# Optimization experiments

Hardware: AMD Instinct MI355X
Metric: run time of the kernel (lower is better)

The kernel has to match this reference:

```python
import jax, jax.numpy as jnp
import numpy as np

NEG_SLOPE = 0.2  # PyG GATConv default negative_slope


def _gat_layer(x, src, dst, n_nodes, W, a_src, a_dst, b):
    # x: [N, din]; src/dst: [E] (self-loops already included)
    h = x @ W                                  # [N, dout]
    s_src = h @ a_src                          # [N]
    s_dst = h @ a_dst                          # [N]
    e = jax.nn.leaky_relu(s_src[src] + s_dst[dst], NEG_SLOPE)  # [E]
    # per-target-node softmax over incoming edges (stable via segment max)
    m = jax.ops.segment_max(e, dst, num_segments=n_nodes)      # [N]
    a = jnp.exp(e - m[dst])                    # [E]
    denom = jax.ops.segment_sum(a, dst, num_segments=n_nodes)  # [N]
    msg = h[src] * a[:, None]                  # [E, dout]
    agg = jax.ops.segment_sum(msg, dst, num_segments=n_nodes)  # [N, dout]
    return agg / denom[:, None] + b


def setup_inputs() -> dict:
    key = jax.random.key(0)
    ks = jax.random.split(key, 16)
    N, E = 100000, 1600000
    in_dim, hid_dim, out_dim = 128, 128, 64
    x = jax.random.normal(ks[0], (N, in_dim), dtype=jnp.float32)
    edge_idx = jax.random.randint(ks[1], (2, E), 0, N, dtype=jnp.int32)

    def lin(k, din, dout):
        return jax.random.normal(k, (din, dout), dtype=jnp.float32) * (1.0 / np.sqrt(din))

    def att(k, dout):
        return jax.random.normal(k, (dout,), dtype=jnp.float32) * (1.0 / np.sqrt(dout))

    return {
        "x": x, "edge_idx": edge_idx,
        "W1": lin(ks[2], in_dim, hid_dim), "as1": att(ks[3], hid_dim), "ad1": att(ks[4], hid_dim), "b1": jnp.zeros((hid_dim,), jnp.float32),
        "W2": lin(ks[5], hid_dim, hid_dim), "as2": att(ks[6], hid_dim), "ad2": att(ks[7], hid_dim), "b2": jnp.zeros((hid_dim,), jnp.float32),
        "W3": lin(ks[8], hid_dim, out_dim), "as3": att(ks[9], out_dim), "ad3": att(ks[10], out_dim), "b3": jnp.zeros((out_dim,), jnp.float32),
    }


def reference(x, edge_idx, W1, as1, ad1, b1, W2, as2, ad2, b2, W3, as3, ad3, b3):
    N = x.shape[0]
    # add self-loops (PyG GATConv default add_self_loops=True)
    loops = jnp.arange(N, dtype=edge_idx.dtype)
    src = jnp.concatenate([edge_idx[0], loops])
    dst = jnp.concatenate([edge_idx[1], loops])
    h = _gat_layer(x, src, dst, N, W1, as1, ad1, b1)
    h = _gat_layer(h, src, dst, N, W2, as2, ad2, b2)
    h = _gat_layer(h, src, dst, N, W3, as3, ad3, b3)
    return jnp.mean(h, axis=-2)  # [out_dim]
```

## Files before the change

kernel.cpp:

```cpp
#include <hip/hip_runtime.h>

static inline int ceil_div(long long a, long long b) { return (int)((a + b - 1) / b); }

typedef __attribute__((ext_vector_type(8))) short bf16x8;
typedef __attribute__((ext_vector_type(4))) float f32x4;

#define TILE 8192
#define BKSH 9

__device__ __forceinline__ float lrelu(float t) { return t > 0.f ? t : 0.2f * t; }

__device__ __forceinline__ void atomAddF(float* p, float v) {
  unsafeAtomicAdd(p, v);
}

__device__ __forceinline__ unsigned int f2bf(float f) {
  unsigned int u = __float_as_uint(f);
  unsigned int r = ((u >> 16) & 1u) + 0x7fffu;
  return (u + r) >> 16;
}

__device__ __forceinline__ void gll16(const void* g, void* l) {
  __builtin_amdgcn_global_load_lds((const __attribute__((address_space(1))) void*)g,
                                   (__attribute__((address_space(3))) void*)l, 16, 0, 0);
}

__global__ void prep(const float* __restrict__ W1, const float* __restrict__ W2,
                     const float* __restrict__ W3, unsigned short* __restrict__ Wt1,
                     unsigned short* __restrict__ Wt2, unsigned short* __restrict__ Wt3,
                     int* __restrict__ tot, float* __restrict__ dout, int NBUK) {
  const int j = blockIdx.x * blockDim.x + threadIdx.x;
  if (j < 40960) {
    const float* W; unsigned short* Wt; int local, DOUTv;
    if (j < 16384)      { W = W1; Wt = Wt1; local = j;          DOUTv = 128; }
    else if (j < 32768) { W = W2; Wt = Wt2; local = j - 16384;  DOUTv = 128; }
    else                { W = W3; Wt = Wt3; local = j - 32768;  DOUTv = 64;  }
    const int k = local / DOUTv, n = local % DOUTv;
    Wt[n * 128 + k] = (unsigned short)f2bf(W[local]);
    return;
  }
  const int z = j - 40960;
  if (z < NBUK) tot[z] = 0;
  else if (z < NBUK + 64) dout[z - NBUK] = 0.f;
}

template<int DOUT, bool XF32>
__launch_bounds__(256)
__global__ void gemm_mfma(const unsigned short* __restrict__ Xb, const float* __restrict__ xf,
                          const unsigned short* __restrict__ Wt,
                          const float* __restrict__ avs, const float* __restrict__ avd,
                          unsigned short* __restrict__ Hb, float* __restrict__ Ss,
                          float* __restrict__ Sd, int N, int RG) {
  constexpr int DIN = 128;
  constexpr int CG = DOUT / 64;
  constexpr int RPB = 4 / CG;
  constexpr int SPSR = (CG == 2) ? RPB : 1;
  constexpr int CHR = DOUT / 4;
  constexpr int SWM = CHR / 8;
  constexpr int XR  = RPB * 64;

  __shared__ float sps[SPSR][2][64], spd[SPSR][2][64];
  __shared__ uint4 smem4[(DOUT + XR) * 16];
  unsigned short* sWt = (unsigned short*)smem4;
  unsigned short* sXb = (unsigned short*)smem4 + DOUT * DIN;
  unsigned int*   sO32 = (unsigned int*)smem4;

  const int tid = threadIdx.x;
  const int wv = tid >> 6;
  const int rgl = wv / CG;
  const int cg  = wv % CG;
  const int rg = blockIdx.x * RPB + rgl;
  const bool active = rg < RG;
  const int lane = tid & 63;
  const int l16 = lane & 15, quad = lane >> 4;
  const int row0 = rg * 64, colw0 = cg * 64;
  const int row0blk = blockIdx.x * XR;

#pragma unroll
  for (int i = 0; i < DOUT / 16; i++) {
    const int r4 = wv * (DOUT / 4) + i * 4;
    const int r = r4 + (lane >> 4);
    const int ch = (lane & 15) ^ (r & 7);
    gll16(Wt + (size_t)r * DIN + ch * 8, sWt + (size_t)r4 * DIN);
  }
  if (XF32) {
    for (int c = tid; c < XR * 16; c += 256) {
      const int row = c >> 4, ch = c & 15;
      int m = row0blk + row; if (m > N - 1) m = N - 1;
      const float4 f0 = *(const float4*)(xf + (size_t)m * DIN + ch * 8);
      const float4 f1 = *(const float4*)(xf + (size_t)m * DIN + ch * 8 + 4);
      uint4 v;
      v.x = f2bf(f0.x) | (f2bf(f0.y) << 16);
      v.y = f2bf(f0.z) | (f2bf(f0.w) << 16);
      v.z = f2bf(f1.x) | (f2bf(f1.y) << 16);
      v.w = f2bf(f1.z) | (f2bf(f1.w) << 16);
      *(uint4*)(sXb + ((row * 16 + (ch ^ (row & 7))) << 3)) = v;
    }
  } else {
#pragma unroll
    for (int i = 0; i < XR / 16; i++) {
      const int r4 = wv * (XR / 4) + i * 4;
      const int lr = r4 + (lane >> 4);
      int m = row0blk + lr; if (m > N - 1) m = N - 1;
      const int ch = (lane & 15) ^ (lr & 7);
      gll16(Xb + (size_t)m * DIN + ch * 8, sXb + (size_t)r4 * DIN);
    }
  }
  __syncthreads();

  f32x4 acc[4][4];
  if (active) {
#pragma unroll
    for (int a = 0; a < 4; a++)
#pragma unroll
      for (int c = 0; c < 4; c++) acc[a][c] = (f32x4)0.f;

#pragma unroll
    for (int kk = 0; kk < 4; kk++) {
      const int chn = kk * 4 + quad;
      const int chs = chn ^ (l16 & 7);
      bf16x8 aw[4], bx[4];
#pragma unroll
      for (int t = 0; t < 4; t++) {
        const int wrow = colw0 + t * 16 + l16;
        aw[t] = *(const bf16x8*)(sWt + ((wrow * 16 + chs) << 3));
      }
#pragma unroll
      for (int t = 0; t < 4; t++) {
        const int xrow = rgl * 64 + t * 16 + l16;
        bx[t] = *(const bf16x8*)(sXb + ((xrow * 16 + chs) << 3));
      }
#pragma unroll
      for (int wt = 0; wt < 4; wt++)
#pragma unroll
        for (int xt = 0; xt < 4; xt++)
          acc[wt][xt] = __builtin_amdgcn_mfma_f32_16x16x32_bf16(aw[wt], bx[xt], acc[wt][xt], 0, 0, 0);
    }

    float4 af[4], df[4];
#pragma unroll
    for (int wt = 0; wt < 4; wt++) {
      af[wt] = *(const float4*)(avs + colw0 + wt * 16 + quad * 4);
      df[wt] = *(const float4*)(avd + colw0 + wt * 16 + quad * 4);
    }
#pragma unroll
    for (int xt = 0; xt < 4; xt++) {
      const int m = row0 + xt * 16 + l16;
      float ps = 0.f, pd = 0.f;
#pragma unroll
      for (int wt = 0; wt < 4; wt++) {
        const f32x4 c = acc[wt][xt];
        ps += c[0]*af[wt].x + c[1]*af[wt].y + c[2]*af[wt].z + c[3]*af[wt].w;
        pd += c[0]*df[wt].x + c[1]*df[wt].y + c[2]*df[wt].z + c[3]*df[wt].w;
      }
      ps += __shfl_xor(ps, 16); ps += __shfl_xor(ps, 32);
      pd += __shfl_xor(pd, 16); pd += __shfl_xor(pd, 32);
      if (quad == 0) {
        if (CG == 2) {
          sps[rgl][cg][xt * 16 + l16] = ps;
          spd[rgl][cg][xt * 16 + l16] = pd;
        } else if (m < N) {
          Ss[m] = ps; Sd[m] = pd;
        }
      }
    }
  }

  __syncthreads();

  if (active) {
#pragma unroll
    for (int xt = 0; xt < 4; xt++) {
      const int rl = rgl * 64 + xt * 16 + l16;
      const int swz = (rl & 7) * SWM;
#pragma unroll
      for (int wt = 0; wt < 4; wt++) {
        const f32x4 c = acc[wt][xt];
        const int ch = (colw0 >> 2) + wt * 4 + quad;
        const int sch = ch ^ swz;
        sO32[rl * (2 * CHR) + 2 * sch]     = f2bf(c[0]) | (f2bf(c[1]) << 16);
        sO32[rl * (2 * CHR) + 2 * sch + 1] = f2bf(c[2]) | (f2bf(c[3]) << 16);
      }
    }
  }
  if (CG == 2 && active && cg == 0) {
    const int m = row0 + lane;
    if (m < N) {
      Ss[m] = sps[rgl][0][lane] + sps[rgl][1][lane];
      Sd[m] = spd[rgl][0][lane] + spd[rgl][1][lane];
    }
  }
  __syncthreads();

  for (int c = tid; c < XR * CHR; c += 256) {
    const int row = c / CHR, ch = c % CHR;
    const int m = row0blk + row;
    if (m < N) {
      const int sch = ch ^ ((row & 7) * SWM);
      uint2 v = make_uint2(sO32[row * (2 * CHR) + 2 * sch],
                           sO32[row * (2 * CHR) + 2 * sch + 1]);
      *(uint2*)(Hb + (size_t)m * DOUT + ch * 4) = v;
    }
  }
}

__launch_bounds__(256)
__global__ void bucket_hist(const int* __restrict__ dstv, int* __restrict__ bh,
                            int* __restrict__ tot, int E, int NBUK) {
  __shared__ int h[256];
  h[threadIdx.x] = 0;
  __syncthreads();
  const int base = blockIdx.x * TILE;
  const int end = min(E, base + TILE);
  for (int i = base + threadIdx.x; i < end; i += 256)
    atomicAdd(&h[dstv[i] >> BKSH], 1);
  __syncthreads();
  if (threadIdx.x < NBUK) {
    const int v = h[threadIdx.x];
    bh[blockIdx.x * NBUK + threadIdx.x] = v;
    if (v) atomicAdd(&tot[threadIdx.x], v);
  }
}

__launch_bounds__(256)
__global__ void scan_fused(int* __restrict__ bh, const int* __restrict__ tot,
                           int* __restrict__ bucketBase, int* __restrict__ rowptr_N,
                           int NBA, int NBUK, int E) {
  __shared__ int sc[256];
  const int t = threadIdx.x;
  if ((int)blockIdx.x < NBUK) {
    const int b = blockIdx.x;
    int carry = 0;
    for (int c0 = 0; c0 < NBA; c0 += 256) {
      const int idx = c0 + t;
      const int v = (idx < NBA) ? bh[idx * NBUK + b] : 0;
      sc[t] = v;
      __syncthreads();
      for (int off = 1; off < 256; off <<= 1) {
        int u = (t >= off) ? sc[t - off] : 0;
        __syncthreads();
        sc[t] += u;
        __syncthreads();
      }
      if (idx < NBA) bh[idx * NBUK + b] = carry + sc[t] - v;
      carry += sc[255];
      __syncthreads();
    }
  } else {
    int carry = 0;
    for (int c0 = 0; c0 < NBUK; c0 += 256) {
      const int idx = c0 + t;
      const int v = (idx < NBUK) ? tot[idx] : 0;
      sc[t] = v;
      __syncthreads();
      for (int off = 1; off < 256; off <<= 1) {
        int u = (t >= off) ? sc[t - off] : 0;
        __syncthreads();
        sc[t] += u;
        __syncthreads();
      }
      if (idx < NBUK) bucketBase[idx] = carry + sc[t] - v;
      carry += sc[255];
      __syncthreads();
    }
    if (t == 0) { bucketBase[NBUK] = E; *rowptr_N = E; }
  }
}

__launch_bounds__(256)
__global__ void bucket_scatter(const int* __restrict__ src, const int* __restrict__ dstv,
                               const int* __restrict__ bh, const int* __restrict__ bucketBase,
                               unsigned int* __restrict__ pairs, int E, int NBUK) {
  __shared__ int ofs[256];
  if (threadIdx.x < NBUK)
    ofs[threadIdx.x] = bh[blockIdx.x * NBUK + threadIdx.x] + bucketBase[threadIdx.x];
  __syncthreads();
  const int base = blockIdx.x * TILE;
  const int end = min(E, base + TILE);
  for (int i = base + threadIdx.x; i < end; i += 256) {
    const int d = dstv[i];
    const int pos = atomicAdd(&ofs[d >> BKSH], 1);
    pairs[pos] = ((unsigned int)src[i] << BKSH) | (unsigned int)(d & ((1 << BKSH) - 1));
  }
}

__launch_bounds__(256)
__global__ void region_build(const unsigned int* __restrict__ pairs,
                             const int* __restrict__ bucketBase,
                             int* __restrict__ rowptr, int* __restrict__ srcs, int N) {
  __shared__ int cnt[512], ofs[512], ps[256];
  const int t = threadIdx.x;
  const int r = blockIdx.x;
  const int p0 = bucketBase[r], p1 = bucketBase[r + 1];
  cnt[t] = 0; cnt[t + 256] = 0;
  __syncthreads();
  for (int i = p0 + t; i < p1; i += 256)
    atomicAdd(&cnt[pairs[i] & 511u], 1);
  __syncthreads();
  const int c0 = cnt[2 * t], c1 = cnt[2 * t + 1];
  const int pr = c0 + c1;
  ps[t] = pr;
  __syncthreads();
  for (int off = 1; off < 256; off <<= 1) {
    int v = (t >= off) ? ps[t - off] : 0;
    __syncthreads();
    ps[t] += v;
    __syncthreads();
  }
  const int pbase = ps[t] - pr;
  ofs[2 * t] = pbase; ofs[2 * t + 1] = pbase + c0;
  __syncthreads();
  {
    const int d0 = (r << BKSH) + t;
    if (d0 < N) rowptr[d0] = p0 + ofs[t];
    const int d1 = (r << BKSH) + t + 256;
    if (d1 < N) rowptr[d1] = p0 + ofs[t + 256];
  }
  __syncthreads();
  for (int i = p0 + t; i < p1; i += 256) {
    const unsigned int w = pairs[i];
    const int pos = atomicAdd(&ofs[w & 511u], 1);
    srcs[p0 + pos] = (int)(w >> BKSH);
  }
}

template<int DOUT, bool OBF, bool MEANRED>
__launch_bounds__(256)
__global__ void node_gather(const int* __restrict__ rowptr, const int* __restrict__ srcs,
                            const float* __restrict__ Ss, const float* __restrict__ Sd,
                            const unsigned short* __restrict__ Hb, const float* __restrict__ b,
                            float* __restrict__ out, unsigned short* __restrict__ outb, int N) {
  constexpr int EPL = DOUT / 16;
  constexpr int WIN = 512;
  __shared__ uint2 s_sw[WIN];
  __shared__ int   rp[17];
  __shared__ float sdv[16];
  __shared__ float s_mean[64];

  const int tid = threadIdx.x;
  const int l16 = tid & 15;
  const int grp = tid >> 4;
  const int node0 = blockIdx.x * 16;
  const int node = node0 + grp;
  const bool nvalid = node < N;

  if (tid < 17) rp[tid] = rowptr[min(node0 + tid, N)];
  if (tid < 16) sdv[tid] = (node0 + tid < N) ? Sd[node0 + tid] : 0.f;
  if (MEANRED && tid < 64) s_mean[tid] = 0.f;
  __syncthreads();

  const int base = rp[0], endE = rp[16];
  const int r0 = rp[grp], r1 = rp[grp + 1];
  const float sd = sdv[grp];

  float acc[EPL];
#pragma unroll
  for (int k = 0; k < EPL; k++) acc[k] = 0.f;
  float lsum = 0.f;
  const int colb = l16 * EPL;

  for (int wb = base; wb < endE; wb += WIN) {
    if (wb != base) __syncthreads();
#pragma unroll
    for (int k0 = 0; k0 < WIN; k0 += 256) {
      const int k = k0 + tid;
      const int i = wb + k;
      if (i < endE) {
        const int s = srcs[i];
        int o = 0;
#pragma unroll
        for (int st = 8; st; st >>= 1)
          if (rp[o + st] <= i) o += st;
        const float w = __expf(lrelu(Ss[s] + sdv[o]));
        s_sw[k] = make_uint2((unsigned)s, __float_as_uint(w));
      }
    }
    __syncthreads();

    const int lo = max(r0, wb), hi = min(r1, wb + WIN);
    const int cnt = hi - lo;
    const int L = lo - wb;
    for (int t = l16; t < cnt; t += 16) lsum += __uint_as_float(s_sw[L + t].y);

    int t = 0;
    for (; t + 8 <= cnt; t += 8) {
      uint2 sw[8];
#pragma unroll
      for (int q = 0; q < 8; q++) sw[q] = s_sw[L + t + q];
      if (EPL == 8) {
        uint4 u[8];
#pragma unroll
        for (int q = 0; q < 8; q++) u[q] = *(const uint4*)(Hb + ((size_t)sw[q].x * DOUT) + colb);
#pragma unroll
        for (int q = 0; q < 8; q++) {
          const float w = __uint_as_float(sw[q].y);
          const unsigned int a[4] = {u[q].x, u[q].y, u[q].z, u[q].w};
#pragma unroll
          for (int k = 0; k < 4; k++) {
            acc[2*k]   += __uint_as_float(a[k] << 16) * w;
            acc[2*k+1] += __uint_as_float(a[k] & 0xffff0000u) * w;
          }
        }
      } else {
        uint2 u[8];
#pragma unroll
        for (int q = 0; q < 8; q++) u[q] = *(const uint2*)(Hb + ((size_t)sw[q].x * DOUT) + colb);
#pragma unroll
        for (int q = 0; q < 8; q++) {
          const float w = __uint_as_float(sw[q].y);
          const unsigned int a[2] = {u[q].x, u[q].y};
#pragma unroll
          for (int k = 0; k < 2; k++) {
            acc[2*k]   += __uint_as_float(a[k] << 16) * w;
            acc[2*k+1] += __uint_as_float(a[k] & 0xffff0000u) * w;
          }
        }
      }
    }
    for (; t < cnt; t += 4) {
      uint2 sw[4]; float wv[4];
#pragma unroll
      for (int q = 0; q < 4; q++) {
        const int tt = min(t + q, cnt - 1);
        sw[q] = s_sw[L + tt];
        wv[q] = (t + q < cnt) ? __uint_as_float(sw[q].y) : 0.f;
      }
      if (EPL == 8) {
        uint4 u[4];
#pragma unroll
        for (int q = 0; q < 4; q++) u[q] = *(const uint4*)(Hb + ((size_t)sw[q].x * DOUT) + colb);
#pragma unroll
        for (int q = 0; q < 4; q++) {
          const unsigned int a[4] = {u[q].x, u[q].y, u[q].z, u[q].w};
#pragma unroll
          for (int k = 0; k < 4; k++) {
            acc[2*k]   += __uint_as_float(a[k] << 16) * wv[q];
            acc[2*k+1] += __uint_as_float(a[k] & 0xffff0000u) * wv[q];
          }
        }
      } else {
        uint2 u[4];
#pragma unroll
        for (int q = 0; q < 4; q++) u[q] = *(const uint2*)(Hb + ((size_t)sw[q].x * DOUT) + colb);
#pragma unroll
        for (int q = 0; q < 4; q++) {
          const unsigned int a[2] = {u[q].x, u[q].y};
#pragma unroll
          for (int k = 0; k < 2; k++) {
            acc[2*k]   += __uint_as_float(a[k] << 16) * wv[q];
            acc[2*k+1] += __uint_as_float(a[k] & 0xffff0000u) * wv[q];
          }
        }
      }
    }
  }

#pragma unroll
  for (int off = 8; off; off >>= 1) lsum += __shfl_xor(lsum, off);

  float wself = 0.f;
  if (nvalid) {
    wself = __expf(lrelu(Ss[node] + sd));
    const unsigned short* pp = Hb + (size_t)node * DOUT + colb;
#pragma unroll
    for (int k = 0; k < EPL / 2; k++) {
      const unsigned int u = ((const unsigned int*)pp)[k];
      acc[2*k]   += __uint_as_float(u << 16) * wself;
      acc[2*k+1] += __uint_as_float(u & 0xffff0000u) * wself;
    }
  }

  if (nvalid) {
    const float inv = 1.f / (lsum + wself);
    float o[EPL];
#pragma unroll
    for (int k = 0; k < EPL; k++) o[k] = acc[k] * inv + b[colb + k];
    if (MEANRED) {
#pragma unroll
      for (int k = 0; k < EPL; k++) atomicAdd(&s_mean[colb + k], o[k]);
    } else if (OBF) {
      if (EPL == 8) {
        uint4 u;
        u.x = f2bf(o[0]) | (f2bf(o[1]) << 16);
        u.y = f2bf(o[2]) | (f2bf(o[3]) << 16);
        u.z = f2bf(o[4]) | (f2bf(o[5]) << 16);
        u.w = f2bf(o[6]) | (f2bf(o[7]) << 16);
        *(uint4*)(outb + (size_t)node * DOUT + colb) = u;
      } else {
        uint2 u;
        u.x = f2bf(o[0]) | (f2bf(o[1]) << 16);
        u.y = f2bf(o[2]) | (f2bf(o[3]) << 16);
        *(uint2*)(outb + (size_t)node * DOUT + colb) = u;
      }
    } else {
      float* op = out + (size_t)node * DOUT + colb;
#pragma unroll
      for (int k = 0; k < EPL; k += 4)
        *(float4*)(op + k) = make_float4(o[k], o[k+1], o[k+2], o[k+3]);
    }
  }
  if (MEANRED) {
    __syncthreads();
    if (tid < 64) out[(size_t)blockIdx.x * 64 + tid] = s_mean[tid];
  }
}

__global__ void mean64(const float* __restrict__ Hf, float* __restrict__ out, int N, float scale) {
  __shared__ float sm[256];
  const int col = threadIdx.x & 63;
  const int seg = threadIdx.x >> 6;
  const int stride = gridDim.x * 4;
  float s = 0.f;
  for (int n = blockIdx.x * 4 + seg; n < N; n += stride) s += Hf[(size_t)n * 64 + col];
  sm[threadIdx.x] = s;
  __syncthreads();
  if (seg == 0) {
    float tot = sm[col] + sm[64 + col] + sm[128 + col] + sm[192 + col];
    atomAddF(&out[col], tot * scale);
  }
}

extern "C" void kernel_launch(void* const* d_in, const int* in_sizes, int n_in,
                              void* d_out, int out_size, void* d_ws, size_t ws_size,
                              hipStream_t stream) {
  const float* x   = (const float*)d_in[0];
  const int*   ei  = (const int*)d_in[1];
  const float* W1  = (const float*)d_in[2];
  const float* as1 = (const float*)d_in[3];
  const float* ad1 = (const float*)d_in[4];
  const float* b1  = (const float*)d_in[5];
  const float* W2  = (const float*)d_in[6];
  const float* as2 = (const float*)d_in[7];
  const float* ad2 = (const float*)d_in[8];
  const float* b2  = (const float*)d_in[9];
  const float* W3  = (const float*)d_in[10];
  const float* as3 = (const float*)d_in[11];
  const float* ad3 = (const float*)d_in[12];
  const float* b3  = (const float*)d_in[13];

  const int N = in_sizes[0] / 128;
  const int E = in_sizes[1] / 2;
  const int* src  = ei;
  const int* dstv = ei + E;
  const int RG = ceil_div(N, 64);
  const int NBA = ceil_div(E, TILE);
  const int NBUK = ceil_div(N, 1 << BKSH);
  const int GG = ceil_div(N, 16);

  float* p = (float*)d_ws;
  float* part = p; p += (size_t)GG * 64;
  float* SsSd = p; p += (size_t)2 * N;
  float* Ss = SsSd, *Sd = SsSd + N;
  unsigned short* Xb = (unsigned short*)p; p += (size_t)N * 64;
  unsigned short* Hb = (unsigned short*)p; p += (size_t)N * 64;
  unsigned short* Wt1 = (unsigned short*)p; p += 128 * 128 / 2;
  unsigned short* Wt2 = (unsigned short*)p; p += 128 * 128 / 2;
  unsigned short* Wt3 = (unsigned short*)p; p += 128 * 64 / 2;
  int* ip = (int*)p;
  int* rowptr     = ip; ip += N + 1;
  int* bh         = ip; ip += (size_t)NBA * NBUK;
  int* tot        = ip; ip += NBUK;
  int* bucketBase = ip; ip += NBUK + 1;
  unsigned int* pairs = (unsigned int*)ip; ip += E;
  int* srcs       = ip; ip += E;

  prep<<<ceil_div(40960 + NBUK + 64, 256), 256, 0, stream>>>(
      W1, W2, W3, Wt1, Wt2, Wt3, tot, (float*)d_out, NBUK);

  bucket_hist<<<NBA, 256, 0, stream>>>(dstv, bh, tot, E, NBUK);
  scan_fused<<<NBUK + 1, 256, 0, stream>>>(bh, tot, bucketBase, rowptr + N, NBA, NBUK, E);
  bucket_scatter<<<NBA, 256, 0, stream>>>(src, dstv, bh, bucketBase, pairs, E, NBUK);
  region_build<<<NBUK, 256, 0, stream>>>(pairs, bucketBase, rowptr, srcs, N);

  gemm_mfma<128, true><<<ceil_div(RG, 2), 256, 0, stream>>>(nullptr, x, Wt1, as1, ad1, Hb, Ss, Sd, N, RG);
  node_gather<128, true, false><<<GG, 256, 0, stream>>>(rowptr, srcs, Ss, Sd, Hb, b1, nullptr, Xb, N);
  gemm_mfma<128, false><<<ceil_div(RG, 2), 256, 0, stream>>>(Xb, nullptr, Wt2, as2, ad2, Hb, Ss, Sd, N, RG);
  node_gather<128, true, false><<<GG, 256, 0, stream>>>(rowptr, srcs, Ss, Sd, Hb, b2, nullptr, Xb, N);
  gemm_mfma<64, false><<<ceil_div(RG, 4), 256, 0, stream>>>(Xb, nullptr, Wt3, as3, ad3, Hb, Ss, Sd, N, RG);
  node_gather<64, false, true><<<GG, 256, 0, stream>>>(rowptr, srcs, Ss, Sd, Hb, b3, part, nullptr, N);

  mean64<<<256, 256, 0, stream>>>(part, (float*)d_out, GG, 1.0f / (float)N);
}
```

Measured before the change: 405.0 us.

## Build CSR with per-node global atomic counts instead of two-pass bucket sort

Replaces the bucketed two-level radix-style CSR construction (per-tile histograms, column scan, pair scatter, per-region local sort) with a simpler scheme. Degrees are counted with global atomics per destination, bucket totals are scanned, rowptr is built per region, and edges are scattered through per-node atomic cursors. This removes the pairs buffer and the multi-block histogram scan. In exchange it adds 1.6M global atomics in two passes with poor locality, and the edge order within each row becomes nondeterministic.

Result: slower. 528.9 us (+30.6%).

```diff
diff --git a/kernel.cpp b/kernel.cpp
--- a/kernel.cpp
+++ b/kernel.cpp
@@ -28,7 +28,8 @@
 __global__ void prep(const float* __restrict__ W1, const float* __restrict__ W2,
                      const float* __restrict__ W3, unsigned short* __restrict__ Wt1,
                      unsigned short* __restrict__ Wt2, unsigned short* __restrict__ Wt3,
-                     int* __restrict__ tot, float* __restrict__ dout, int NBUK) {
+                     int* __restrict__ cnt, int* __restrict__ tot, float* __restrict__ dout,
+                     int CNTSZ, int NBUK) {
   const int j = blockIdx.x * blockDim.x + threadIdx.x;
   if (j < 40960) {
     const float* W; unsigned short* Wt; int local, DOUTv;
@@ -39,9 +40,12 @@
     Wt[n * 128 + k] = (unsigned short)f2bf(W[local]);
     return;
   }
-  const int z = j - 40960;
-  if (z < NBUK) tot[z] = 0;
-  else if (z < NBUK + 64) dout[z - NBUK] = 0.f;
+  int z = j - 40960;
+  if (z < CNTSZ) { cnt[z] = 0; return; }
+  z -= CNTSZ;
+  if (z < NBUK) { tot[z] = 0; return; }
+  z -= NBUK;
+  if (z < 64) dout[z] = 0.f;
 }
 
 template<int DOUT, bool XF32>
@@ -205,99 +209,57 @@
 }
 
 __launch_bounds__(256)
-__global__ void bucket_hist(const int* __restrict__ dstv, int* __restrict__ bh,
+__global__ void bucket_hist(const int* __restrict__ dstv, int* __restrict__ cnt,
                             int* __restrict__ tot, int E, int NBUK) {
   __shared__ int h[256];
   h[threadIdx.x] = 0;
-  __syncthreads();
-  const int base = blockIdx.x * TILE;
-  const int end = min(E, base + TILE);
-  for (int i = base + threadIdx.x; i < end; i += 256)
-    atomicAdd(&h[dstv[i] >> BKSH], 1);
-  __syncthreads();
-  if (threadIdx.x < NBUK) {
-    const int v = h[threadIdx.x];
-    bh[blockIdx.x * NBUK + threadIdx.x] = v;
-    if (v) atomicAdd(&tot[threadIdx.x], v);
-  }
-}
-
-__launch_bounds__(256)
-__global__ void scan_fused(int* __restrict__ bh, const int* __restrict__ tot,
-                           int* __restrict__ bucketBase, int* __restrict__ rowptr_N,
-                           int NBA, int NBUK, int E) {
-  __shared__ int sc[256];
-  const int t = threadIdx.x;
-  if ((int)blockIdx.x < NBUK) {
-    const int b = blockIdx.x;
-    int carry = 0;
-    for (int c0 = 0; c0 < NBA; c0 += 256) {
-      const int idx = c0 + t;
-      const int v = (idx < NBA) ? bh[idx * NBUK + b] : 0;
-      sc[t] = v;
-      __syncthreads();
-      for (int off = 1; off < 256; off <<= 1) {
-        int u = (t >= off) ? sc[t - off] : 0;
-        __syncthreads();
-        sc[t] += u;
-        __syncthreads();
-      }
-      if (idx < NBA) bh[idx * NBUK + b] = carry + sc[t] - v;
-      carry += sc[255];
-      __syncthreads();
-    }
-  } else {
-    int carry = 0;
-    for (int c0 = 0; c0 < NBUK; c0 += 256) {
-      const int idx = c0 + t;
-      const int v = (idx < NBUK) ? tot[idx] : 0;
-      sc[t] = v;
-      __syncthreads();
-      for (int off = 1; off < 256; off <<= 1) {
-        int u = (t >= off) ? sc[t - off] : 0;
-        __syncthreads();
-        sc[t] += u;
-        __syncthreads();
-      }
-      if (idx < NBUK) bucketBase[idx] = carry + sc[t] - v;
-      carry += sc[255];
-      __syncthreads();
-    }
-    if (t == 0) { bucketBase[NBUK] = E; *rowptr_N = E; }
-  }
-}
-
-__launch_bounds__(256)
-__global__ void bucket_scatter(const int* __restrict__ src, const int* __restrict__ dstv,
-                               const int* __restrict__ bh, const int* __restrict__ bucketBase,
-                               unsigned int* __restrict__ pairs, int E, int NBUK) {
-  __shared__ int ofs[256];
-  if (threadIdx.x < NBUK)
-    ofs[threadIdx.x] = bh[blockIdx.x * NBUK + threadIdx.x] + bucketBase[threadIdx.x];
   __syncthreads();
   const int base = blockIdx.x * TILE;
   const int end = min(E, base + TILE);
   for (int i = base + threadIdx.x; i < end; i += 256) {
     const int d = dstv[i];
-    const int pos = atomicAdd(&ofs[d >> BKSH], 1);
-    pairs[pos] = ((unsigned int)src[i] << BKSH) | (unsigned int)(d & ((1 << BKSH) - 1));
+    atomicAdd(&h[d >> BKSH], 1);
+    atomicAdd(&cnt[d], 1);
+  }
+  __syncthreads();
+  if (threadIdx.x < NBUK) {
+    const int v = h[threadIdx.x];
+    if (v) atomicAdd(&tot[threadIdx.x], v);
   }
 }
 
 __launch_bounds__(256)
-__global__ void region_build(const unsigned int* __restrict__ pairs,
-                             const int* __restrict__ bucketBase,
-                             int* __restrict__ rowptr, int* __restrict__ srcs, int N) {
-  __shared__ int cnt[512], ofs[512], ps[256];
+__global__ void scan_tot(const int* __restrict__ tot, int* __restrict__ bucketBase,
+                         int* __restrict__ rowptr_N, int NBUK, int E) {
+  __shared__ int sc[256];
+  const int t = threadIdx.x;
+  int carry = 0;
+  for (int c0 = 0; c0 < NBUK; c0 += 256) {
+    const int idx = c0 + t;
+    const int v = (idx < NBUK) ? tot[idx] : 0;
+    sc[t] = v;
+    __syncthreads();
+    for (int off = 1; off < 256; off <<= 1) {
+      int u = (t >= off) ? sc[t - off] : 0;
+      __syncthreads();
+      sc[t] += u;
+      __syncthreads();
+    }
+    if (idx < NBUK) bucketBase[idx] = carry + sc[t] - v;
+    carry += sc[255];
+    __syncthreads();
+  }
+  if (t == 0) { bucketBase[NBUK] = E; *rowptr_N = E; }
+}
+
+__launch_bounds__(256)
+__global__ void rowptr_build(const int* __restrict__ cnt, const int* __restrict__ bucketBase,
+                             int* __restrict__ rowptr, int* __restrict__ wcnt, int N) {
+  __shared__ int ps[256];
   const int t = threadIdx.x;
   const int r = blockIdx.x;
-  const int p0 = bucketBase[r], p1 = bucketBase[r + 1];
-  cnt[t] = 0; cnt[t + 256] = 0;
-  __syncthreads();
-  for (int i = p0 + t; i < p1; i += 256)
-    atomicAdd(&cnt[pairs[i] & 511u], 1);
-  __syncthreads();
-  const int c0 = cnt[2 * t], c1 = cnt[2 * t + 1];
+  const int base = r << BKSH;
+  const int c0 = cnt[base + 2 * t], c1 = cnt[base + 2 * t + 1];
   const int pr = c0 + c1;
   ps[t] = pr;
   __syncthreads();
@@ -307,20 +269,19 @@
     ps[t] += v;
     __syncthreads();
   }
-  const int pbase = ps[t] - pr;
-  ofs[2 * t] = pbase; ofs[2 * t + 1] = pbase + c0;
-  __syncthreads();
-  {
-    const int d0 = (r << BKSH) + t;
-    if (d0 < N) rowptr[d0] = p0 + ofs[t];
-    const int d1 = (r << BKSH) + t + 256;
-    if (d1 < N) rowptr[d1] = p0 + ofs[t + 256];
-  }
-  __syncthreads();
-  for (int i = p0 + t; i < p1; i += 256) {
-    const unsigned int w = pairs[i];
-    const int pos = atomicAdd(&ofs[w & 511u], 1);
-    srcs[p0 + pos] = (int)(w >> BKSH);
+  const int pbase = bucketBase[r] + ps[t] - pr;
+  const int d0 = base + 2 * t, d1 = d0 + 1;
+  if (d0 < N) { rowptr[d0] = pbase;      wcnt[d0] = pbase; }
+  if (d1 < N) { rowptr[d1] = pbase + c0; wcnt[d1] = pbase + c0; }
+}
+
+__launch_bounds__(256)
+__global__ void edge_scatter(const int* __restrict__ src, const int* __restrict__ dstv,
+                             int* __restrict__ wcnt, int* __restrict__ srcs, int E) {
+  const int i = blockIdx.x * blockDim.x + threadIdx.x;
+  if (i < E) {
+    const int pos = atomicAdd(&wcnt[dstv[i]], 1);
+    srcs[pos] = src[i];
   }
 }
 
@@ -545,6 +506,7 @@
   const int RG = ceil_div(N, 64);
   const int NBA = ceil_div(E, TILE);
   const int NBUK = ceil_div(N, 1 << BKSH);
+  const int CNTSZ = NBUK << BKSH;
   const int GG = ceil_div(N, 16);
 
   float* p = (float*)d_ws;
@@ -558,19 +520,19 @@
   unsigned short* Wt3 = (unsigned short*)p; p += 128 * 64 / 2;
   int* ip = (int*)p;
   int* rowptr     = ip; ip += N + 1;
-  int* bh         = ip; ip += (size_t)NBA * NBUK;
+  int* cnt        = ip; ip += CNTSZ;
+  int* wcnt       = ip; ip += CNTSZ;
   int* tot        = ip; ip += NBUK;
   int* bucketBase = ip; ip += NBUK + 1;
-  unsigned int* pairs = (unsigned int*)ip; ip += E;
   int* srcs       = ip; ip += E;
 
-  prep<<<ceil_div(40960 + NBUK + 64, 256), 256, 0, stream>>>(
-      W1, W2, W3, Wt1, Wt2, Wt3, tot, (float*)d_out, NBUK);
-
-  bucket_hist<<<NBA, 256, 0, stream>>>(dstv, bh, tot, E, NBUK);
-  scan_fused<<<NBUK + 1, 256, 0, stream>>>(bh, tot, bucketBase, rowptr + N, NBA, NBUK, E);
-  bucket_scatter<<<NBA, 256, 0, stream>>>(src, dstv, bh, bucketBase, pairs, E, NBUK);
-  region_build<<<NBUK, 256, 0, stream>>>(pairs, bucketBase, rowptr, srcs, N);
+  prep<<<ceil_div((long long)40960 + CNTSZ + NBUK + 64, 256), 256, 0, stream>>>(
+      W1, W2, W3, Wt1, Wt2, Wt3, cnt, tot, (float*)d_out, CNTSZ, NBUK);
+
+  bucket_hist<<<NBA, 256, 0, stream>>>(dstv, cnt, tot, E, NBUK);
+  scan_tot<<<1, 256, 0, stream>>>(tot, bucketBase, rowptr + N, NBUK, E);
+  rowptr_build<<<NBUK, 256, 0, stream>>>(cnt, bucketBase, rowptr, wcnt, N);
+  edge_scatter<<<ceil_div(E, 256), 256, 0, stream>>>(src, dstv, wcnt, srcs, E);
 
   gemm_mfma<128, true><<<ceil_div(RG, 2), 256, 0, stream>>>(nullptr, x, Wt1, as1, ad1, Hb, Ss, Sd, N, RG);
   node_gather<128, true, false><<<GG, 256, 0, stream>>>(rowptr, srcs, Ss, Sd, Hb, b1, nullptr, Xb, N);
```
